# Kernel optimization log

Hardware: AMD Instinct MI355X
Metric: run time of the kernel (lower is better)

The kernel has to match this reference:

```python
import jax, jax.numpy as jnp
import numpy as np

N_NODES = 100000
N_EDGES = 1600000
D_IN = 512
D_HID = 128
N_CLASSES = 100


def _gcn_norm(edge_index, n_nodes):
    # Add self loops and compute symmetric normalization D^{-1/2} (A+I) D^{-1/2}
    sl = jnp.arange(n_nodes, dtype=edge_index.dtype)
    src = jnp.concatenate([edge_index[0], sl])
    dst = jnp.concatenate([edge_index[1], sl])
    deg = jax.ops.segment_sum(jnp.ones_like(dst, dtype=jnp.float32), dst,
                              num_segments=n_nodes)
    dinv = jnp.where(deg > 0, jax.lax.rsqrt(deg), 0.0)
    norm = dinv[src] * dinv[dst]  # [E + N]
    return src, dst, norm


def _gcn_layer(x, W, b, src, dst, norm, n_nodes):
    h = x @ W                                  # [N, d_out] (transform first, like PyG GCNConv)
    msg = h[src] * norm[:, None]               # [E+N, d_out] gather + scale
    out = jax.ops.segment_sum(msg, dst, num_segments=n_nodes)  # scatter-add
    return out + b


def setup_inputs() -> dict:
    key = jax.random.key(0)
    ks = jax.random.split(key, 6)
    x = jax.random.normal(ks[0], (N_NODES, D_IN), dtype=jnp.float32)
    edge_index = jax.random.randint(ks[1], (2, N_EDGES), 0, N_NODES, dtype=jnp.int64)
    W1 = jax.random.normal(ks[2], (D_IN, D_HID), dtype=jnp.float32) * (1.0 / np.sqrt(D_IN))
    b1 = jnp.zeros((D_HID,), dtype=jnp.float32)
    W2 = jax.random.normal(ks[3], (D_HID, N_CLASSES), dtype=jnp.float32) * (1.0 / np.sqrt(D_HID))
    b2 = jnp.zeros((N_CLASSES,), dtype=jnp.float32)
    return {"x": x, "edge_index": edge_index, "W1": W1, "b1": b1, "W2": W2, "b2": b2}


def reference(x, edge_index, W1, b1, W2, b2):
    n_nodes = x.shape[0]
    src, dst, norm = _gcn_norm(edge_index, n_nodes)
    h = jax.nn.relu(_gcn_layer(x, W1, b1, src, dst, norm, n_nodes))
    logits = _gcn_layer(h, W2, b2, src, dst, norm, n_nodes)
    return jax.nn.log_softmax(logits, axis=-1)
```

## Files before the change

### kernel.cpp

```cpp
#include <hip/hip_runtime.h>
#include <math.h>

typedef __attribute__((ext_vector_type(8))) short short8;
typedef __attribute__((ext_vector_type(4))) float f32x4;
typedef _Float16 half8 __attribute__((ext_vector_type(8)));
typedef __fp16 fp16x2 __attribute__((ext_vector_type(2)));
typedef unsigned int uint;

__device__ inline uint f2bf(float f) {
    uint u = __float_as_uint(f);
    return (u + 0x7fffu + ((u >> 16) & 1u)) >> 16;
}
__device__ inline uint pack2(float lo, float hi) { return f2bf(lo) | (f2bf(hi) << 16); }
__device__ inline float bflo(uint u) { return __uint_as_float(u << 16); }
__device__ inline float bfhi(uint u) { return __uint_as_float(u & 0xffff0000u); }
__device__ inline uint cvtpk(float lo, float hi) {
    uint r;
    asm("v_cvt_pk_bf16_f32 %0, %1, %2" : "=v"(r) : "v"(lo), "v"(hi));
    return r;
}
__device__ inline uint pkh(float lo, float hi) {
    union { fp16x2 h; uint u; } c;
    c.h = __builtin_amdgcn_cvt_pkrtz(lo, hi);
    return c.u;
}
__device__ inline void gload16(const void* g, void* l) {
    __builtin_amdgcn_global_load_lds(
        (const __attribute__((address_space(1))) void*)g,
        (__attribute__((address_space(3))) void*)l, 16, 0, 0);
}

__global__ void k_prep(const int* __restrict__ dst, int E, int nbE, int* __restrict__ cnt,
                       const float* __restrict__ W1, ushort* __restrict__ w1frag,
                       const float* __restrict__ W2, const float* __restrict__ b2,
                       ushort* __restrict__ w2frag, float* __restrict__ b2pad) {
    int bid = blockIdx.x;
    if (bid < nbE) {
        int i = bid * 256 + threadIdx.x;
        if (i < E) atomicAdd(&cnt[dst[i]], 1);
        return;
    }
    bid -= nbE;
    if (bid < 32) {
        int tid = bid * 256 + threadIdx.x;
        int ks = tid >> 9;
        int t = (tid >> 6) & 7;
        int l = tid & 63;
        int kbase = ks * 32 + (l >> 4) * 8;
        int c = t * 16 + (l & 15);
#pragma unroll
        for (int j = 0; j < 8; j++) {
            float v = W1[(size_t)(kbase + j) * 128 + c];
            union { _Float16 h; ushort u; } cv;
            cv.h = (_Float16)v;
            w1frag[(size_t)tid * 8 + j] = cv.u;
        }
        return;
    }
    bid -= 32;
    {
        int tid = bid * 256 + threadIdx.x;
        if (tid < 1792) {
            int q = tid / 448;
            int t = (tid >> 6) % 7;
            int l = tid & 63;
            int kbase = q * 32 + (l >> 4) * 8;
            int c = t * 16 + (l & 15);
#pragma unroll
            for (int j = 0; j < 8; j++) {
                float v = (c < 100) ? W2[(kbase + j) * 100 + c] : 0.f;
                w2frag[(size_t)tid * 8 + j] = (ushort)f2bf(v);
            }
        } else if (tid < 1792 + 112) {
            int c = tid - 1792;
            b2pad[c] = (c < 100) ? b2[c] : -1e30f;
        }
    }
}

__global__ __launch_bounds__(512) void k_scan1(const int* __restrict__ cnt, int* __restrict__ rp,
                                               int* __restrict__ partials, float* __restrict__ dinv,
                                               int N) {
    __shared__ int s[512];
    int i = blockIdx.x * 512 + threadIdx.x;
    int v = (i < N) ? cnt[i] : 0;
    if (i < N) dinv[i] = rsqrtf((float)(v + 1));
    s[threadIdx.x] = v;
    __syncthreads();
    for (int d = 1; d < 512; d <<= 1) {
        int t = (threadIdx.x >= d) ? s[threadIdx.x - d] : 0;
        __syncthreads();
        s[threadIdx.x] += t;
        __syncthreads();
    }
    if (i < N) rp[i] = s[threadIdx.x] - v;
    if (threadIdx.x == 511) partials[blockIdx.x] = s[511];
}

__global__ __launch_bounds__(256) void k_scan2(int* __restrict__ partials, int nb) {
    __shared__ int s[256];
    int carry = 0;
    for (int base = 0; base < nb; base += 256) {
        int i = base + threadIdx.x;
        int v = (i < nb) ? partials[i] : 0;
        s[threadIdx.x] = v;
        __syncthreads();
        for (int d = 1; d < 256; d <<= 1) {
            int t = (threadIdx.x >= d) ? s[threadIdx.x - d] : 0;
            __syncthreads();
            s[threadIdx.x] += t;
            __syncthreads();
        }
        if (i < nb) partials[i] = carry + s[threadIdx.x] - v;
        carry += s[255];
        __syncthreads();
    }
}

__global__ __launch_bounds__(512) void k_scan3(int* __restrict__ rp, const int* __restrict__ partials,
                                               int N, int E) {
    int i = blockIdx.x * 512 + threadIdx.x;
    if (i < N) rp[i] += partials[blockIdx.x];
    if (i == 0) rp[N] = E;
}

__global__ void k_fill(const int* __restrict__ src, const int* __restrict__ dst, int E,
                       const int* __restrict__ rp, int* __restrict__ cursor,
                       const float* __restrict__ dinv, float2* __restrict__ colw) {
    int i = blockIdx.x * 256 + threadIdx.x;
    if (i < E) {
        int d = dst[i];
        int s = src[i];
        int pos = rp[d] + atomicAdd(&cursor[d], 1);
        colw[pos] = make_float2(__int_as_float(s), dinv[s]);
    }
}

__global__ __launch_bounds__(512) void k_gemm1(const float* __restrict__ x,
                                               const uint4* __restrict__ w1f,
                                               uint* __restrict__ h1, int N) {
    __shared__ __align__(16) char lds[49152];
    int tid = threadIdx.x, wv = tid >> 6, l = tid & 63;
    int cl = l & 15, kg = l >> 4;
    int row0 = blockIdx.x * 64;
    int rq = wv & 3, chalf = wv >> 2;

    int xr = tid >> 3, xs = tid & 7;
    int xrg = row0 + xr; if (xrg >= N) xrg = N - 1;
    const float* xsrc = x + (size_t)xrg * 512 + xs * 8;

    auto stageB = [&](int c) {
        char* bbase = lds + 16384 + (c & 1) * 16384;
        const char* bsrc = (const char*)w1f + (size_t)c * 16384;
#pragma unroll
        for (int i = 0; i < 2; i++) {
            int s = i * 512 + tid;
            gload16(bsrc + (size_t)s * 16, bbase + (size_t)(s - l) * 16);
        }
    };

    float4 f0, f1;
    auto loadx = [&](int c) {
        const float* p = xsrc + c * 64;
        f0 = *(const float4*)p;
        f1 = *(const float4*)(p + 4);
    };
    auto writex = [&](int c) {
        char* xb = lds + (c & 1) * 8192;
        uint4 v;
        v.x = pkh(f0.x, f0.y);
        v.y = pkh(f0.z, f0.w);
        v.z = pkh(f1.x, f1.y);
        v.w = pkh(f1.z, f1.w);
        *(uint4*)(xb + xr * 128 + ((xs ^ (xr & 7)) * 16)) = v;
    };

    f32x4 acc[4];
#pragma unroll
    for (int t = 0; t < 4; t++) acc[t] = (f32x4){0.f, 0.f, 0.f, 0.f};

    union U { uint4 u4; half8 h8; };
    int arow = rq * 16 + cl;

    loadx(0);
    stageB(0);
    writex(0);
    __syncthreads();

    for (int c = 0; c < 8; c++) {
        if (c < 7) { loadx(c + 1); stageB(c + 1); }
        const char* xb = lds + (c & 1) * 8192;
        const char* bb = lds + 16384 + (c & 1) * 16384;
#pragma unroll
        for (int k2 = 0; k2 < 2; k2++) {
            U A;
            A.u4 = *(const uint4*)(xb + arow * 128 + (((k2 * 4 + kg) ^ (arow & 7)) * 16));
#pragma unroll
            for (int tt = 0; tt < 4; tt++) {
                U B;
                B.u4 = *(const uint4*)(bb + (size_t)(((k2 * 8 + chalf * 4 + tt) * 64 + l)) * 16);
                acc[tt] = __builtin_amdgcn_mfma_f32_16x16x32_f16(A.h8, B.h8, acc[tt], 0, 0, 0);
            }
        }
        if (c < 7) writex(c + 1);
        __syncthreads();
    }

    uint* hsp = (uint*)lds + (size_t)wv * (16 * 33);
#pragma unroll
    for (int tt = 0; tt < 4; tt++)
#pragma unroll
        for (int r = 0; r < 4; r++) {
            float mine = acc[tt][r];
            float other = __shfl_xor(mine, 1, 64);
            if ((cl & 1) == 0)
                hsp[(kg * 4 + r) * 33 + tt * 8 + (cl >> 1)] = cvtpk(mine, other);
        }
#pragma unroll
    for (int p = 0; p < 8; p++) {
        int it = p * 2 + (l >> 5);
        int gr = row0 + rq * 16 + it;
        if (gr < N) h1[(size_t)gr * 64 + chalf * 32 + (l & 31)] = hsp[it * 33 + (l & 31)];
    }
}

template <bool RELU_BIAS>
__global__ __launch_bounds__(256) void k_agg(const uint* __restrict__ h, const float* __restrict__ dinv,
                                             const int* __restrict__ rp, const float2* __restrict__ colw,
                                             const float* __restrict__ bias, uint* __restrict__ outb, int N) {
    int wave = threadIdx.x >> 6, lane = threadIdx.x & 63;
    int v = blockIdx.x * 4 + wave;
    if (v >= N) return;
    float dv = dinv[v];
    float wself = dv * dv;
    uint us = h[(size_t)v * 64 + lane];
    float acc0 = bflo(us) * wself;
    float acc1 = bfhi(us) * wself;
    int e0 = rp[v], e1 = rp[v + 1];
    int i = e0;
    for (; i + 8 <= e1; i += 8) {
        float2 q[8];
        uint u[8];
#pragma unroll
        for (int j = 0; j < 8; j++) q[j] = colw[i + j];
#pragma unroll
        for (int j = 0; j < 8; j++) u[j] = h[(size_t)__float_as_int(q[j].x) * 64 + lane];
#pragma unroll
        for (int j = 0; j < 8; j++) {
            float w = q[j].y * dv;
            acc0 = fmaf(bflo(u[j]), w, acc0);
            acc1 = fmaf(bfhi(u[j]), w, acc1);
        }
    }
    if (i + 4 <= e1) {
        float2 q[4];
        uint u[4];
#pragma unroll
        for (int j = 0; j < 4; j++) q[j] = colw[i + j];
#pragma unroll
        for (int j = 0; j < 4; j++) u[j] = h[(size_t)__float_as_int(q[j].x) * 64 + lane];
#pragma unroll
        for (int j = 0; j < 4; j++) {
            float w = q[j].y * dv;
            acc0 = fmaf(bflo(u[j]), w, acc0);
            acc1 = fmaf(bfhi(u[j]), w, acc1);
        }
        i += 4;
    }
    for (; i < e1; i++) {
        float2 q = colw[i];
        uint u = h[(size_t)__float_as_int(q.x) * 64 + lane];
        float w = q.y * dv;
        acc0 = fmaf(bflo(u), w, acc0);
        acc1 = fmaf(bfhi(u), w, acc1);
    }
    if (RELU_BIAS) {
        float2 b = *(const float2*)&bias[2 * lane];
        acc0 = fmaxf(acc0 + b.x, 0.f);
        acc1 = fmaxf(acc1 + b.y, 0.f);
    }
    outb[(size_t)v * 64 + lane] = pack2(acc0, acc1);
}

__global__ __launch_bounds__(256) void k_out_mfma(const uint* __restrict__ g2u,
                                                  const uint4* __restrict__ w2fragG,
                                                  const float* __restrict__ b2pad,
                                                  float* __restrict__ out, int N) {
    __shared__ uint4 w2s[1792];
    __shared__ float b2s[112];
    int tid = threadIdx.x;
    for (int i = tid; i < 1792; i += 256) w2s[i] = w2fragG[i];
    if (tid < 112) b2s[tid] = b2pad[tid];
    __syncthreads();

    int w = tid >> 6, l = tid & 63;
    int v0 = blockIdx.x * 128 + w * 32;
    int cl = l & 15, gq = l >> 4;

    f32x4 acc[2][7];
#pragma unroll
    for (int m = 0; m < 2; m++)
#pragma unroll
        for (int t = 0; t < 7; t++) acc[m][t] = (f32x4){0.f, 0.f, 0.f, 0.f};

    union U { uint4 u4; short8 s8; };

#pragma unroll
    for (int q = 0; q < 4; q++) {
        short8 afr[2];
#pragma unroll
        for (int m = 0; m < 2; m++) {
            int rv = v0 + m * 16 + cl;
            if (rv >= N) rv = N - 1;
            U a;
            a.u4 = *(const uint4*)&g2u[(size_t)rv * 64 + q * 16 + gq * 4];
            afr[m] = a.s8;
        }
#pragma unroll
        for (int t = 0; t < 7; t++) {
            U b;
            b.u4 = w2s[(q * 7 + t) * 64 + l];
            acc[0][t] = __builtin_amdgcn_mfma_f32_16x16x32_bf16(afr[0], b.s8, acc[0][t], 0, 0, 0);
            acc[1][t] = __builtin_amdgcn_mfma_f32_16x16x32_bf16(afr[1], b.s8, acc[1][t], 0, 0, 0);
        }
    }

    float bsv[7];
#pragma unroll
    for (int t = 0; t < 7; t++) bsv[t] = b2s[t * 16 + cl];

#pragma unroll
    for (int m = 0; m < 2; m++) {
#pragma unroll
        for (int r = 0; r < 4; r++) {
            int row = v0 + m * 16 + gq * 4 + r;
            float lg[7];
#pragma unroll
            for (int t = 0; t < 7; t++) lg[t] = acc[m][t][r] + bsv[t];
            float mx = lg[0];
#pragma unroll
            for (int t = 1; t < 7; t++) mx = fmaxf(mx, lg[t]);
            mx = fmaxf(mx, __shfl_xor(mx, 1, 64));
            mx = fmaxf(mx, __shfl_xor(mx, 2, 64));
            mx = fmaxf(mx, __shfl_xor(mx, 4, 64));
            mx = fmaxf(mx, __shfl_xor(mx, 8, 64));
            float s = 0.f;
#pragma unroll
            for (int t = 0; t < 7; t++) s += __expf(lg[t] - mx);
            s += __shfl_xor(s, 1, 64);
            s += __shfl_xor(s, 2, 64);
            s += __shfl_xor(s, 4, 64);
            s += __shfl_xor(s, 8, 64);
            float lse = mx + __logf(s);
            if (row < N) {
#pragma unroll
                for (int t = 0; t < 7; t++) {
                    int c = t * 16 + cl;
                    if (c < 100) out[(size_t)row * 100 + c] = lg[t] - lse;
                }
            }
        }
    }
}

extern "C" void kernel_launch(void* const* d_in, const int* in_sizes, int n_in,
                              void* d_out, int out_size, void* d_ws, size_t ws_size,
                              hipStream_t stream) {
    const float* x  = (const float*)d_in[0];
    const int*   ei = (const int*)d_in[1];
    const float* W1 = (const float*)d_in[2];
    const float* b1 = (const float*)d_in[3];
    const float* W2 = (const float*)d_in[4];
    const float* b2 = (const float*)d_in[5];
    float* out = (float*)d_out;

    int N = in_sizes[0] / 512;
    int E = in_sizes[1] / 2;
    const int* srcI = ei;
    const int* dstI = ei + E;

    char* wsb = (char*)d_ws;
    size_t off = 0;
    auto alloc = [&](size_t bytes) {
        void* p = wsb + off;
        off = (off + bytes + 255) & ~(size_t)255;
        return p;
    };
    int*    cnt      = (int*)alloc((size_t)N * 4);
    int*    cursor   = (int*)alloc((size_t)N * 4);
    float*  dinv     = (float*)alloc((size_t)N * 4);
    int*    rp       = (int*)alloc((size_t)(N + 1) * 4);
    int*    partials = (int*)alloc(1024 * 4);
    ushort* w1f      = (ushort*)alloc(8192 * 8 * 2);
    ushort* w2frag   = (ushort*)alloc(1792 * 8 * 2);
    float*  b2pad    = (float*)alloc(112 * 4);
    float2* colw     = (float2*)alloc((size_t)E * 8);
    uint*   h1       = (uint*)alloc((size_t)N * 64 * 4);
    uint*   a1       = (uint*)alloc((size_t)N * 64 * 4);
    uint*   g2       = h1;

    hipMemsetAsync(cnt, 0, (size_t)2 * (((size_t)N * 4 + 255) & ~(size_t)255), stream);

    int nbE = (E + 255) / 256;
    k_prep<<<nbE + 40, 256, 0, stream>>>(dstI, E, nbE, cnt, W1, w1f, W2, b2, w2frag, b2pad);
    int nb = (N + 511) / 512;
    k_scan1<<<nb, 512, 0, stream>>>(cnt, rp, partials, dinv, N);
    k_scan2<<<1, 256, 0, stream>>>(partials, nb);
    k_scan3<<<nb, 512, 0, stream>>>(rp, partials, N, E);
    k_fill<<<(E + 255) / 256, 256, 0, stream>>>(srcI, dstI, E, rp, cursor, dinv, colw);

    k_gemm1<<<(N + 63) / 64, 512, 0, stream>>>(x, (const uint4*)w1f, h1, N);
    k_agg<true><<<(N + 3) / 4, 256, 0, stream>>>(h1, dinv, rp, colw, b1, a1, N);
    k_agg<false><<<(N + 3) / 4, 256, 0, stream>>>(a1, dinv, rp, colw, nullptr, g2, N);
    k_out_mfma<<<(N + 127) / 128, 256, 0, stream>>>(g2, (const uint4*)w2frag, b2pad, out, N);
}
```

Before: 371.3 us.

## Merge scan passes and co-schedule CSR fill with first GEMM

k_scan2 is removed. Each k_scan3 block now computes its own prefix by reducing all preceding partials itself, which saves one serial single-block launch. The CSR fill kernel and the first GEMM are merged into one launch, with a block-index split between them, so the atomic scatter and the dense GEMM can overlap on the GPU. In exchange, fill blocks now reserve 48KB of LDS, which may limit how many run at once, and k_scan3 does redundant reduction work that grows with block index.

Result: no change. 367.1 us (-1.1%).

```diff
diff --git a/kernel.cpp b/kernel.cpp
--- a/kernel.cpp
+++ b/kernel.cpp
@@ -97,52 +97,45 @@
     if (threadIdx.x == 511) partials[blockIdx.x] = s[511];
 }
 
-__global__ __launch_bounds__(256) void k_scan2(int* __restrict__ partials, int nb) {
-    __shared__ int s[256];
-    int carry = 0;
-    for (int base = 0; base < nb; base += 256) {
-        int i = base + threadIdx.x;
-        int v = (i < nb) ? partials[i] : 0;
-        s[threadIdx.x] = v;
-        __syncthreads();
-        for (int d = 1; d < 256; d <<= 1) {
-            int t = (threadIdx.x >= d) ? s[threadIdx.x - d] : 0;
-            __syncthreads();
-            s[threadIdx.x] += t;
-            __syncthreads();
-        }
-        if (i < nb) partials[i] = carry + s[threadIdx.x] - v;
-        carry += s[255];
-        __syncthreads();
-    }
-}
-
 __global__ __launch_bounds__(512) void k_scan3(int* __restrict__ rp, const int* __restrict__ partials,
                                                int N, int E) {
-    int i = blockIdx.x * 512 + threadIdx.x;
-    if (i < N) rp[i] += partials[blockIdx.x];
+    __shared__ int sw[8];
+    int bid = blockIdx.x, tid = threadIdx.x;
+    int acc = 0;
+    for (int i = tid; i < bid; i += 512) acc += partials[i];
+#pragma unroll
+    for (int d = 32; d > 0; d >>= 1) acc += __shfl_xor(acc, d, 64);
+    if ((tid & 63) == 0) sw[tid >> 6] = acc;
+    __syncthreads();
+    int tot = 0;
+#pragma unroll
+    for (int w = 0; w < 8; w++) tot += sw[w];
+    int i = bid * 512 + tid;
+    if (i < N) rp[i] += tot;
     if (i == 0) rp[N] = E;
 }
 
-__global__ void k_fill(const int* __restrict__ src, const int* __restrict__ dst, int E,
-                       const int* __restrict__ rp, int* __restrict__ cursor,
-                       const float* __restrict__ dinv, float2* __restrict__ colw) {
-    int i = blockIdx.x * 256 + threadIdx.x;
-    if (i < E) {
-        int d = dst[i];
-        int s = src[i];
-        int pos = rp[d] + atomicAdd(&cursor[d], 1);
-        colw[pos] = make_float2(__int_as_float(s), dinv[s]);
-    }
-}
-
-__global__ __launch_bounds__(512) void k_gemm1(const float* __restrict__ x,
-                                               const uint4* __restrict__ w1f,
-                                               uint* __restrict__ h1, int N) {
+__global__ __launch_bounds__(512) void k_fillgemm1(const int* __restrict__ src, const int* __restrict__ dst,
+                                                   int E, int nbF, const int* __restrict__ rp,
+                                                   int* __restrict__ cursor, const float* __restrict__ dinv,
+                                                   float2* __restrict__ colw,
+                                                   const float* __restrict__ x,
+                                                   const uint4* __restrict__ w1f,
+                                                   uint* __restrict__ h1, int N) {
     __shared__ __align__(16) char lds[49152];
+    if (blockIdx.x < nbF) {
+        int i = blockIdx.x * 512 + threadIdx.x;
+        if (i < E) {
+            int d = dst[i];
+            int s = src[i];
+            int pos = rp[d] + atomicAdd(&cursor[d], 1);
+            colw[pos] = make_float2(__int_as_float(s), dinv[s]);
+        }
+        return;
+    }
     int tid = threadIdx.x, wv = tid >> 6, l = tid & 63;
     int cl = l & 15, kg = l >> 4;
-    int row0 = blockIdx.x * 64;
+    int row0 = (blockIdx.x - nbF) * 64;
     int rq = wv & 3, chalf = wv >> 2;
 
     int xr = tid >> 3, xs = tid & 7;
@@ -405,11 +398,13 @@
     k_prep<<<nbE + 40, 256, 0, stream>>>(dstI, E, nbE, cnt, W1, w1f, W2, b2, w2frag, b2pad);
     int nb = (N + 511) / 512;
     k_scan1<<<nb, 512, 0, stream>>>(cnt, rp, partials, dinv, N);
-    k_scan2<<<1, 256, 0, stream>>>(partials, nb);
     k_scan3<<<nb, 512, 0, stream>>>(rp, partials, N, E);
-    k_fill<<<(E + 255) / 256, 256, 0, stream>>>(srcI, dstI, E, rp, cursor, dinv, colw);
-
-    k_gemm1<<<(N + 63) / 64, 512, 0, stream>>>(x, (const uint4*)w1f, h1, N);
+
+    int nbF = (E + 511) / 512;
+    int nbG = (N + 63) / 64;
+    k_fillgemm1<<<nbF + nbG, 512, 0, stream>>>(srcI, dstI, E, nbF, rp, cursor, dinv, colw,
+                                               x, (const uint4*)w1f, h1, N);
+
     k_agg<true><<<(N + 3) / 4, 256, 0, stream>>>(h1, dinv, rp, colw, b1, a1, N);
     k_agg<false><<<(N + 3) / 4, 256, 0, stream>>>(a1, dinv, rp, colw, nullptr, g2, N);
     k_out_mfma<<<(N + 127) / 128, 256, 0, stream>>>(g2, (const uint4*)w2frag, b2pad, out, N);
```
